# Kernel tuning notes

Measured on AMD Instinct MI355X. Metric: run time of the kernel, lower is better.

## Reference

```python
import jax, jax.numpy as jnp
import numpy as np

N_HEADS, D_MODEL, D_HEAD = 16, 1024, 64
EPSILON = -100000.0  # module uses -1e5, not -inf
INIT_STD = 0.02


def setup_inputs() -> dict:
    key = jax.random.key(0)
    ks = jax.random.split(key, 5)
    B, S = 4, 2048
    x = jax.random.normal(ks[0], (B, S, D_MODEL), dtype=jnp.float32)
    W_Q = INIT_STD * jax.random.normal(ks[1], (N_HEADS, D_MODEL, D_HEAD), dtype=jnp.float32)
    W_K = INIT_STD * jax.random.normal(ks[2], (N_HEADS, D_MODEL, D_HEAD), dtype=jnp.float32)
    W_V = INIT_STD * jax.random.normal(ks[3], (N_HEADS, D_MODEL, D_HEAD), dtype=jnp.float32)
    W_O = INIT_STD * jax.random.normal(ks[4], (N_HEADS, D_HEAD, D_MODEL), dtype=jnp.float32)
    b_Q = jnp.zeros((N_HEADS, D_HEAD), jnp.float32)
    b_K = jnp.zeros((N_HEADS, D_HEAD), jnp.float32)
    b_V = jnp.zeros((N_HEADS, D_HEAD), jnp.float32)
    b_O = jnp.zeros((D_MODEL,), jnp.float32)
    return {"normalized_resid_pre": x, "W_Q": W_Q, "b_Q": b_Q, "W_K": W_K,
            "b_K": b_K, "W_V": W_V, "b_V": b_V, "W_O": W_O, "b_O": b_O}


def reference(normalized_resid_pre, W_Q, b_Q, W_K, b_K, W_V, b_V, W_O, b_O):
    x = normalized_resid_pre  # [b, s, e]
    q = jnp.einsum('bse,neh->bsnh', x, W_Q) + b_Q
    k = jnp.einsum('bse,neh->bsnh', x, W_K) + b_K
    v = jnp.einsum('bse,neh->bsnh', x, W_V) + b_V
    scores = jnp.einsum('bqnh,bknh->bnqk', q, k) / jnp.sqrt(jnp.float32(D_HEAD))
    sq, sk = scores.shape[-2], scores.shape[-1]
    causal = jnp.triu(jnp.ones((sq, sk), bool), k=1)  # True above diagonal
    scores = jnp.where(causal, jnp.float32(EPSILON), scores)
    probs = jax.nn.softmax(scores, axis=-1)
    z = jnp.einsum('bnqk,bknh->bqnh', probs, v)
    # sum over heads of per-head output projection + bias
    attn_out = jnp.einsum('bqnh,nhe->bqe', z, W_O) + b_O
    return attn_out
```

## Files before the change

kernel.cpp:

```cpp
#include <hip/hip_runtime.h>


typedef __attribute__((ext_vector_type(8))) short short8;
typedef __attribute__((ext_vector_type(4))) float floatx4;

#define SCL 0.1803368801111244f

__device__ __forceinline__ unsigned short f2bf(float f) {
  unsigned int x = __float_as_uint(f);
  x += 0x7fffu + ((x >> 16) & 1u);
  return (unsigned short)(x >> 16);
}

__device__ __forceinline__ void gload_lds16(const unsigned short* g, unsigned short* lds) {
  __builtin_amdgcn_global_load_lds(
      (const __attribute__((address_space(1))) void*)g,
      (__attribute__((address_space(3))) void*)lds, 16, 0, 0);
}

__global__ __launch_bounds__(256) void prep_kernel(
    const float* __restrict__ X,  unsigned short* __restrict__ Xb,
    const float* __restrict__ Wq, const float* __restrict__ Wk,
    const float* __restrict__ Wv, unsigned short* __restrict__ Bt,
    const float* __restrict__ Wo, unsigned short* __restrict__ Wt)
{
  __shared__ unsigned short T[64 * 72];
  const int bid = blockIdx.x, t = threadIdx.x;
  if (bid < 8192) {
    int idx = ((bid << 8) + t) << 2;
    float4 f = *(const float4*)(X + idx);
    unsigned short u[4] = { f2bf(f.x), f2bf(f.y), f2bf(f.z), f2bf(f.w) };
    *(uint2*)(Xb + idx) = *(uint2*)u;
  } else if (bid < 8960) {
    int b2 = bid - 8192;
    int e0 = (b2 & 15) << 6, nn = (b2 >> 4) & 15, proj = b2 >> 8;
    const float* W = (proj == 0) ? Wq : (proj == 1) ? Wk : Wv;
    const float* src = W + ((size_t)nn << 16) + ((size_t)e0 << 6);
#pragma unroll
    for (int rnd = 0; rnd < 4; ++rnd) {
      int off = (rnd << 10) + (t << 2);
      float4 f = *(const float4*)(src + off);
      int r = off >> 6, h = off & 63;
      T[r * 72 + h]     = f2bf(f.x);
      T[r * 72 + h + 1] = f2bf(f.y);
      T[r * 72 + h + 2] = f2bf(f.z);
      T[r * 72 + h + 3] = f2bf(f.w);
    }
    __syncthreads();
    const int h = t >> 2, ck = t & 3;
    size_t orow = ((size_t)((proj << 10) + (nn << 6) + h) << 10) + e0 + (ck << 4);
#pragma unroll
    for (int g = 0; g < 2; ++g) {
      unsigned short v[8];
#pragma unroll
      for (int j = 0; j < 8; ++j) v[j] = T[((ck << 4) + (g << 3) + j) * 72 + h];
      *(int4*)(Bt + orow + (g << 3)) = *(int4*)v;
    }
  } else {
    int b2 = bid - 8960;
    int e0 = (b2 & 15) << 6, k0 = (b2 >> 4) << 6;
#pragma unroll
    for (int rnd = 0; rnd < 4; ++rnd) {
      int r = (rnd << 4) + (t >> 4);
      int c = (t & 15) << 2;
      float4 f = *(const float4*)(Wo + ((size_t)(k0 + r) << 10) + e0 + c);
      T[r * 72 + c]     = f2bf(f.x);
      T[r * 72 + c + 1] = f2bf(f.y);
      T[r * 72 + c + 2] = f2bf(f.z);
      T[r * 72 + c + 3] = f2bf(f.w);
    }
    __syncthreads();
    const int i = t >> 2, ck = t & 3;
    size_t orow = ((size_t)(e0 + i) << 10) + k0 + (ck << 4);
#pragma unroll
    for (int g = 0; g < 2; ++g) {
      unsigned short v[8];
#pragma unroll
      for (int j = 0; j < 8; ++j) v[j] = T[((ck << 4) + (g << 3) + j) * 72 + i];
      *(int4*)(Wt + orow + (g << 3)) = *(int4*)v;
    }
  }
}

template <int MODE>
__global__ __launch_bounds__(256) void gemm128_kernel(
    const unsigned short* __restrict__ A,
    const unsigned short* __restrict__ Bt,
    const float* __restrict__ b0, const float* __restrict__ b1,
    const float* __restrict__ b2,
    unsigned short* __restrict__ Oq, unsigned short* __restrict__ Ok,
    unsigned short* __restrict__ Ov, float* __restrict__ Of)
{
  const int K = 1024;
  __shared__ __align__(16) unsigned short As[8192];
  __shared__ __align__(16) unsigned short Bs[8192];
  const int tid = threadIdx.x;
  const int l   = tid & 63, w = tid >> 6;
  const int l15 = l & 15,  lg = l >> 4;
  const int mo  = (w >> 1) << 6, no = (w & 1) << 6;
  const int m0  = blockIdx.y << 7, n0 = blockIdx.x << 7;
  const int srow = l >> 3;
  const int gblk = ((l & 7) ^ srow) << 3;
  const int rsw  = l15 & 7;

  floatx4 acc[4][4];
#pragma unroll
  for (int i = 0; i < 4; ++i)
#pragma unroll
    for (int j = 0; j < 4; ++j) acc[i][j] = (floatx4){0.f, 0.f, 0.f, 0.f};

  for (int k0 = 0; k0 < K; k0 += 64) {
    __syncthreads();
#pragma unroll
    for (int s = 0; s < 4; ++s) {
      const int br = (s << 5) + (w << 3);
      gload_lds16(A  + (size_t)(m0 + br + srow) * K + k0 + gblk, &As[br << 6]);
      gload_lds16(Bt + (size_t)(n0 + br + srow) * K + k0 + gblk, &Bs[br << 6]);
    }
    __syncthreads();
#pragma unroll
    for (int kh = 0; kh < 2; ++kh) {
      const int bo = (((kh << 2) + lg) ^ rsw) << 3;
      short8 af[4], bf[4];
#pragma unroll
      for (int mc = 0; mc < 4; ++mc)
        af[mc] = *(const short8*)&As[((mo + (mc << 4) + l15) << 6) + bo];
#pragma unroll
      for (int nc = 0; nc < 4; ++nc)
        bf[nc] = *(const short8*)&Bs[((no + (nc << 4) + l15) << 6) + bo];
#pragma unroll
      for (int mc = 0; mc < 4; ++mc)
#pragma unroll
        for (int nc = 0; nc < 4; ++nc)
          acc[mc][nc] = __builtin_amdgcn_mfma_f32_16x16x32_bf16(af[mc], bf[nc], acc[mc][nc], 0, 0, 0);
    }
  }

#pragma unroll
  for (int nc = 0; nc < 4; ++nc) {
    int c = n0 + no + (nc << 4) + l15;
    if (MODE == 1) {
      float bv = b0[c];
#pragma unroll
      for (int mc = 0; mc < 4; ++mc)
#pragma unroll
        for (int r = 0; r < 4; ++r) {
          int m = m0 + mo + (mc << 4) + (lg << 2) + r;
          Of[((size_t)m << 10) + c] = acc[mc][nc][r] + bv;
        }
    } else {
      int proj = c >> 10, cc = c & 1023;
      int hn = cc >> 6, h = cc & 63;
      const float* bp = (proj == 0) ? b0 : (proj == 1) ? b1 : b2;
      float bv = bp[cc];
      float sc = (proj == 0) ? SCL : 1.0f;
      if (proj < 2) {
        unsigned short* O = (proj == 0) ? Oq : Ok;
#pragma unroll
        for (int mc = 0; mc < 4; ++mc)
#pragma unroll
          for (int r = 0; r < 4; ++r) {
            int m = m0 + mo + (mc << 4) + (lg << 2) + r;
            int bb = m >> 11, ss = m & 2047;
            O[((((size_t)(bb << 4) + hn) << 11) + ss) * 64 + h] = f2bf((acc[mc][nc][r] + bv) * sc);
          }
      } else {
#pragma unroll
        for (int mc = 0; mc < 4; ++mc) {
          int m = m0 + mo + (mc << 4) + (lg << 2);
          int bb = m >> 11, ss = m & 2047;
          unsigned short p0 = f2bf(acc[mc][nc][0] + bv);
          unsigned short p1 = f2bf(acc[mc][nc][1] + bv);
          unsigned short p2 = f2bf(acc[mc][nc][2] + bv);
          unsigned short p3 = f2bf(acc[mc][nc][3] + bv);
          uint2 pk;
          pk.x = (unsigned int)p0 | ((unsigned int)p1 << 16);
          pk.y = (unsigned int)p2 | ((unsigned int)p3 << 16);
          *(uint2*)&Ov[((((size_t)(bb << 4) + hn) << 6) + h) * 2048 + ss] = pk;
        }
      }
    }
  }
}

__global__ __launch_bounds__(128) void flash5_kernel(
    const unsigned short* __restrict__ Q,
    const unsigned short* __restrict__ K,
    const unsigned short* __restrict__ Vt,
    unsigned short* __restrict__ Z)
{
  __shared__ __align__(16) unsigned short Ks[4096];
  __shared__ __align__(16) unsigned short Vs[4096];
  __shared__ __align__(16) unsigned short Ps[2 * 2304];

  const int tid = threadIdx.x;
  const int l   = tid & 63, w = tid >> 6;
  const int l15 = l & 15,  lg = l >> 4;
  const int x    = blockIdx.x;
  const int pidx = (x >> 3) & 15;
  const int head = ((x & 7) << 3) + (x >> 7);
  const int n = head & 15, b = head >> 4;
  const size_t hoff = (size_t)head << 17;
  const unsigned short* Qh = Q + hoff;
  const unsigned short* Kh = K + hoff;
  const unsigned short* Vh = Vt + hoff;
  unsigned short* Psw = Ps + w * 2304;

  const int srow8 = l >> 3;
  const int sblk8 = ((l & 7) ^ srow8) << 3;
  const int swz   = l15 & 7;
  const int bo0   = (lg ^ swz) << 3;
  const int bo1   = ((4 + lg) ^ swz) << 3;

  short8 onef;
#pragma unroll
  for (int i = 0; i < 8; ++i) onef[i] = (short)0x3F80;

  for (int half = 0; half < 2; ++half) {
    const int qt  = half ? pidx : (31 - pidx);
    const int q0w = (qt << 6) + (w << 5);

    short8 qf[2][2];
#pragma unroll
    for (int qc = 0; qc < 2; ++qc)
#pragma unroll
      for (int dh = 0; dh < 2; ++dh)
        qf[qc][dh] = *(const short8*)(Qh + (size_t)(q0w + (qc << 4) + l15) * 64 + (dh << 5) + (lg << 3));

    floatx4 acc_o[2][4], acc_l[2];
#pragma unroll
    for (int qc = 0; qc < 2; ++qc) {
      acc_l[qc] = (floatx4){0.f, 0.f, 0.f, 0.f};
#pragma unroll
      for (int dc = 0; dc < 4; ++dc) acc_o[qc][dc] = (floatx4){0.f, 0.f, 0.f, 0.f};
    }

    const int nkt = qt + 1;
    for (int kt = 0; kt < nkt; ++kt) {
      const int k0 = kt << 6;
      __syncthreads();
#pragma unroll
      for (int j = 0; j < 4; ++j) {
        const int s = (w << 2) + j;
        gload_lds16(Kh + (size_t)(k0 + (s << 3) + srow8) * 64 + sblk8, &Ks[s << 9]);
        gload_lds16(Vh + (size_t)((s << 3) + srow8) * 2048 + k0 + sblk8, &Vs[s << 9]);
      }
      __syncthreads();

      floatx4 s0[4], s1[4];
#pragma unroll
      for (int mc = 0; mc < 4; ++mc) {
        s0[mc] = (floatx4){0.f, 0.f, 0.f, 0.f};
        s1[mc] = (floatx4){0.f, 0.f, 0.f, 0.f};
      }
#pragma unroll
      for (int dh = 0; dh < 2; ++dh) {
        const int bo = dh ? bo1 : bo0;
#pragma unroll
        for (int mc = 0; mc < 4; ++mc) {
          short8 ak = *(const short8*)&Ks[(((mc << 4) + l15) << 6) + bo];
          s0[mc] = __builtin_amdgcn_mfma_f32_16x16x32_bf16(ak, qf[0][dh], s0[mc], 0, 0, 0);
          s1[mc] = __builtin_amdgcn_mfma_f32_16x16x32_bf16(ak, qf[1][dh], s1[mc], 0, 0, 0);
        }
      }

      const bool needmask = (k0 + 63 > q0w);
#pragma unroll
      for (int qc = 0; qc < 2; ++qc) {
        const int qg = q0w + (qc << 4) + l15;
#pragma unroll
        for (int mc = 0; mc < 4; ++mc) {
          float p[4];
#pragma unroll
          for (int r = 0; r < 4; ++r) {
            float e = exp2f(qc ? s1[mc][r] : s0[mc][r]);
            if (needmask) {
              int key = k0 + (mc << 4) + (lg << 2) + r;
              e = (key > qg) ? 0.f : e;
            }
            p[r] = e;
          }
          uint2 pk;
          pk.x = (__float_as_uint(p[1]) & 0xFFFF0000u) | (__float_as_uint(p[0]) >> 16);
          pk.y = (__float_as_uint(p[3]) & 0xFFFF0000u) | (__float_as_uint(p[2]) >> 16);
          *(uint2*)&Psw[((qc << 4) + l15) * 72 + (mc << 4) + (lg << 2)] = pk;
        }
      }

      short8 pa[2][2];
#pragma unroll
      for (int qc = 0; qc < 2; ++qc)
#pragma unroll
        for (int kc = 0; kc < 2; ++kc)
          pa[qc][kc] = *(const short8*)&Psw[((qc << 4) + l15) * 72 + (kc << 5) + (lg << 3)];
#pragma unroll
      for (int kc = 0; kc < 2; ++kc) {
        const int bo = kc ? bo1 : bo0;
#pragma unroll
        for (int dc = 0; dc < 4; ++dc) {
          short8 vb = *(const short8*)&Vs[(((dc << 4) + l15) << 6) + bo];
          acc_o[0][dc] = __builtin_amdgcn_mfma_f32_16x16x32_bf16(pa[0][kc], vb, acc_o[0][dc], 0, 0, 0);
          acc_o[1][dc] = __builtin_amdgcn_mfma_f32_16x16x32_bf16(pa[1][kc], vb, acc_o[1][dc], 0, 0, 0);
        }
        acc_l[0] = __builtin_amdgcn_mfma_f32_16x16x32_bf16(pa[0][kc], onef, acc_l[0], 0, 0, 0);
        acc_l[1] = __builtin_amdgcn_mfma_f32_16x16x32_bf16(pa[1][kc], onef, acc_l[1], 0, 0, 0);
      }
    }

#pragma unroll
    for (int qc = 0; qc < 2; ++qc) {
      floatx4 inv;
#pragma unroll
      for (int r = 0; r < 4; ++r) inv[r] = 1.f / acc_l[qc][r];
#pragma unroll
      for (int dc = 0; dc < 4; ++dc)
#pragma unroll
        for (int r = 0; r < 4; ++r) {
          int qg = q0w + (qc << 4) + (lg << 2) + r;
          Z[(((size_t)b << 11) + qg) * 1024 + (n << 6) + (dc << 4) + l15] =
              f2bf(acc_o[qc][dc][r] * inv[r]);
        }
    }
  }
}

extern "C" void kernel_launch(void* const* d_in, const int* in_sizes, int n_in,
                              void* d_out, int out_size, void* d_ws, size_t ws_size,
                              hipStream_t stream) {
  const float* x   = (const float*)d_in[0];
  const float* W_Q = (const float*)d_in[1];
  const float* b_Q = (const float*)d_in[2];
  const float* W_K = (const float*)d_in[3];
  const float* b_K = (const float*)d_in[4];
  const float* W_V = (const float*)d_in[5];
  const float* b_V = (const float*)d_in[6];
  const float* W_O = (const float*)d_in[7];
  const float* b_O = (const float*)d_in[8];
  float* out = (float*)d_out;

  unsigned short* ws    = (unsigned short*)d_ws;
  unsigned short* BtQKV = ws;
  unsigned short* Wo_t  = BtQKV + (3u << 20);
  unsigned short* Xb    = Wo_t + (1u << 20);
  unsigned short* Qb    = Xb + (8u << 20);
  unsigned short* Kb    = Qb + (8u << 20);
  unsigned short* Vtb   = Kb + (8u << 20);
  unsigned short* Zb    = Vtb + (8u << 20);

  prep_kernel<<<9216, 256, 0, stream>>>(x, Xb, W_Q, W_K, W_V, BtQKV, W_O, Wo_t);

  gemm128_kernel<0><<<dim3(24, 64), 256, 0, stream>>>(
      Xb, BtQKV, b_Q, b_K, b_V, Qb, Kb, Vtb, nullptr);

  flash5_kernel<<<1024, 128, 0, stream>>>(Qb, Kb, Vtb, Zb);

  gemm128_kernel<1><<<dim3(8, 64), 256, 0, stream>>>(
      Zb, Wo_t, b_O, nullptr, nullptr, nullptr, nullptr, nullptr, out);
}
```

Before: 283.4 us.

## Double-buffer K/V tiles in flash attention and swizzle P scratch layout

The flash attention kernel now double-buffers K and V tiles in LDS, prefetching the next tile (including the first tile of the second half) while computing on the current one. This replaces the two barriers per iteration with one waitcnt plus barrier at the end. The P scratch buffer moves from padded rows to an XOR-swizzled layout, and s_setprio brackets the MFMA sections. LDS use roughly doubles, which may reduce occupancy.

```diff
diff --git a/kernel.cpp b/kernel.cpp
--- a/kernel.cpp
+++ b/kernel.cpp
@@ -183,15 +183,15 @@
   }
 }
 
-__global__ __launch_bounds__(128) void flash5_kernel(
+__global__ __launch_bounds__(128) void flash6_kernel(
     const unsigned short* __restrict__ Q,
     const unsigned short* __restrict__ K,
     const unsigned short* __restrict__ Vt,
     unsigned short* __restrict__ Z)
 {
-  __shared__ __align__(16) unsigned short Ks[4096];
-  __shared__ __align__(16) unsigned short Vs[4096];
-  __shared__ __align__(16) unsigned short Ps[2 * 2304];
+  __shared__ __align__(16) unsigned short Ks[8192];
+  __shared__ __align__(16) unsigned short Vs[8192];
+  __shared__ __align__(16) unsigned short Ps[4096];
 
   const int tid = threadIdx.x;
   const int l   = tid & 63, w = tid >> 6;
@@ -204,7 +204,7 @@
   const unsigned short* Qh = Q + hoff;
   const unsigned short* Kh = K + hoff;
   const unsigned short* Vh = Vt + hoff;
-  unsigned short* Psw = Ps + w * 2304;
+  unsigned short* Psw = Ps + (w << 11);
 
   const int srow8 = l >> 3;
   const int sblk8 = ((l & 7) ^ srow8) << 3;
@@ -212,10 +212,28 @@
   const int bo0   = (lg ^ swz) << 3;
   const int bo1   = ((4 + lg) ^ swz) << 3;
 
+  int pwofs[4], profs[2];
+#pragma unroll
+  for (int mc = 0; mc < 4; ++mc)
+    pwofs[mc] = ((((mc << 1) + (lg >> 1)) ^ swz) << 3) + ((lg & 1) << 2);
+#pragma unroll
+  for (int kc = 0; kc < 2; ++kc)
+    profs[kc] = (((kc << 2) + lg) ^ swz) << 3;
+
   short8 onef;
 #pragma unroll
   for (int i = 0; i < 8; ++i) onef[i] = (short)0x3F80;
 
+#pragma unroll
+  for (int j = 0; j < 4; ++j) {
+    const int s = (w << 2) + j;
+    gload_lds16(Kh + (size_t)((s << 3) + srow8) * 64 + sblk8, &Ks[s << 9]);
+    gload_lds16(Vh + (size_t)((s << 3) + srow8) * 2048 + sblk8, &Vs[s << 9]);
+  }
+  asm volatile("s_waitcnt vmcnt(0)" ::: "memory");
+  __builtin_amdgcn_s_barrier();
+
+  int buf = 0;
   for (int half = 0; half < 2; ++half) {
     const int qt  = half ? pidx : (31 - pidx);
     const int q0w = (qt << 6) + (w << 5);
@@ -237,15 +255,19 @@
 
     const int nkt = qt + 1;
     for (int kt = 0; kt < nkt; ++kt) {
+      int nk0 = (kt + 1 < nkt) ? ((kt + 1) << 6) : (half == 0 ? 0 : -1);
+      if (nk0 >= 0) {
+        const int nb = (buf ^ 1) << 12;
+#pragma unroll
+        for (int j = 0; j < 4; ++j) {
+          const int s = (w << 2) + j;
+          gload_lds16(Kh + (size_t)(nk0 + (s << 3) + srow8) * 64 + sblk8, &Ks[nb + (s << 9)]);
+          gload_lds16(Vh + (size_t)((s << 3) + srow8) * 2048 + nk0 + sblk8, &Vs[nb + (s << 9)]);
+        }
+      }
+
       const int k0 = kt << 6;
-      __syncthreads();
-#pragma unroll
-      for (int j = 0; j < 4; ++j) {
-        const int s = (w << 2) + j;
-        gload_lds16(Kh + (size_t)(k0 + (s << 3) + srow8) * 64 + sblk8, &Ks[s << 9]);
-        gload_lds16(Vh + (size_t)((s << 3) + srow8) * 2048 + k0 + sblk8, &Vs[s << 9]);
-      }
-      __syncthreads();
+      const int cb = buf << 12;
 
       floatx4 s0[4], s1[4];
 #pragma unroll
@@ -253,21 +275,24 @@
         s0[mc] = (floatx4){0.f, 0.f, 0.f, 0.f};
         s1[mc] = (floatx4){0.f, 0.f, 0.f, 0.f};
       }
+      __builtin_amdgcn_s_setprio(1);
 #pragma unroll
       for (int dh = 0; dh < 2; ++dh) {
         const int bo = dh ? bo1 : bo0;
 #pragma unroll
         for (int mc = 0; mc < 4; ++mc) {
-          short8 ak = *(const short8*)&Ks[(((mc << 4) + l15) << 6) + bo];
+          short8 ak = *(const short8*)&Ks[cb + (((mc << 4) + l15) << 6) + bo];
           s0[mc] = __builtin_amdgcn_mfma_f32_16x16x32_bf16(ak, qf[0][dh], s0[mc], 0, 0, 0);
           s1[mc] = __builtin_amdgcn_mfma_f32_16x16x32_bf16(ak, qf[1][dh], s1[mc], 0, 0, 0);
         }
       }
+      __builtin_amdgcn_s_setprio(0);
 
       const bool needmask = (k0 + 63 > q0w);
 #pragma unroll
       for (int qc = 0; qc < 2; ++qc) {
         const int qg = q0w + (qc << 4) + l15;
+        const int rbase = ((qc << 4) + l15) << 6;
 #pragma unroll
         for (int mc = 0; mc < 4; ++mc) {
           float p[4];
@@ -283,28 +308,36 @@
           uint2 pk;
           pk.x = (__float_as_uint(p[1]) & 0xFFFF0000u) | (__float_as_uint(p[0]) >> 16);
           pk.y = (__float_as_uint(p[3]) & 0xFFFF0000u) | (__float_as_uint(p[2]) >> 16);
-          *(uint2*)&Psw[((qc << 4) + l15) * 72 + (mc << 4) + (lg << 2)] = pk;
+          *(uint2*)&Psw[rbase + pwofs[mc]] = pk;
         }
       }
 
       short8 pa[2][2];
 #pragma unroll
-      for (int qc = 0; qc < 2; ++qc)
+      for (int qc = 0; qc < 2; ++qc) {
+        const int rbase = ((qc << 4) + l15) << 6;
 #pragma unroll
         for (int kc = 0; kc < 2; ++kc)
-          pa[qc][kc] = *(const short8*)&Psw[((qc << 4) + l15) * 72 + (kc << 5) + (lg << 3)];
+          pa[qc][kc] = *(const short8*)&Psw[rbase + profs[kc]];
+      }
+      __builtin_amdgcn_s_setprio(1);
 #pragma unroll
       for (int kc = 0; kc < 2; ++kc) {
         const int bo = kc ? bo1 : bo0;
 #pragma unroll
         for (int dc = 0; dc < 4; ++dc) {
-          short8 vb = *(const short8*)&Vs[(((dc << 4) + l15) << 6) + bo];
+          short8 vb = *(const short8*)&Vs[cb + (((dc << 4) + l15) << 6) + bo];
           acc_o[0][dc] = __builtin_amdgcn_mfma_f32_16x16x32_bf16(pa[0][kc], vb, acc_o[0][dc], 0, 0, 0);
           acc_o[1][dc] = __builtin_amdgcn_mfma_f32_16x16x32_bf16(pa[1][kc], vb, acc_o[1][dc], 0, 0, 0);
         }
         acc_l[0] = __builtin_amdgcn_mfma_f32_16x16x32_bf16(pa[0][kc], onef, acc_l[0], 0, 0, 0);
         acc_l[1] = __builtin_amdgcn_mfma_f32_16x16x32_bf16(pa[1][kc], onef, acc_l[1], 0, 0, 0);
       }
+      __builtin_amdgcn_s_setprio(0);
+
+      asm volatile("s_waitcnt vmcnt(0)" ::: "memory");
+      __builtin_amdgcn_s_barrier();
+      buf ^= 1;
     }
 
 #pragma unroll
@@ -352,7 +385,7 @@
   gemm128_kernel<0><<<dim3(24, 64), 256, 0, stream>>>(
       Xb, BtQKV, b_Q, b_K, b_V, Qb, Kb, Vtb, nullptr);
 
-  flash5_kernel<<<1024, 128, 0, stream>>>(Qb, Kb, Vtb, Zb);
+  flash6_kernel<<<1024, 128, 0, stream>>>(Qb, Kb, Vtb, Zb);
 
   gemm128_kernel<1><<<dim3(8, 64), 256, 0, stream>>>(
       Zb, Wo_t, b_O, nullptr, nullptr, nullptr, nullptr, nullptr, out);
```

After: 276.0 us. -2.6%, faster.
